# Kernel tuning notes

Hardware: AMD Instinct MI355X
Metric: run time of the kernel (lower is better)

The kernel has to match this reference:

```python
import jax, jax.numpy as jnp
import numpy as np

GROUP_SIZE = 128


def setup_inputs() -> dict:
    key = jax.random.key(0)
    k1, k2, k3 = jax.random.split(key, 3)
    B, S, IN, OUT = 4, 8192, 1024, 1024
    x = jax.random.normal(k1, (B, S, IN), dtype=jnp.float32)
    weight = jax.random.normal(k2, (OUT, IN), dtype=jnp.float32) * 0.02
    bias = jax.random.normal(k3, (OUT,), dtype=jnp.float32) * 0.01
    return {"x": x, "weight": weight, "bias": bias}


def reference(x, weight, bias):
    """Quantized int8 path: quantize() + _forward_int8 of OneBitLinear.

    - weights binarized to +/-1 int8 (sign, with 0 -> -1, matching
      sign().clamp(min=0) bit packing then 2*bit-1)
    - per-group weight scales = group absmax, stored fp16 (as in quantize())
    - activations dynamically quantized per-token to int8
    - int32-accumulated GEMM, rescaled by x_scale * mean group scale per row
    """
    out_f, in_f = weight.shape
    ng = in_f // GROUP_SIZE
    w_g = weight.reshape(out_f, ng, GROUP_SIZE)
    # per-group absmax scales, cast fp16 -> fp32 to mimic fp16 storage
    scales = jnp.maximum(jnp.max(jnp.abs(w_g), axis=-1), 1e-8)
    scales = scales.astype(jnp.float16).astype(jnp.float32)  # [O, ng]
    # +/-1 int8 weights (sign>0 -> +1, else -1; zero maps to -1 like the packer)
    w_int8 = jnp.where(weight > 0, 1, -1).astype(jnp.int8)  # [O, I]

    # dynamic per-token activation quantization
    x_f = x.reshape(-1, in_f)  # [BT, I]
    x_scale = jnp.maximum(jnp.max(jnp.abs(x_f), axis=1, keepdims=True), 1e-8) / 127.0
    x_int8 = jnp.clip(jnp.round(x_f / x_scale), -128, 127).astype(jnp.int8)

    # int8 GEMM with int32 accumulation
    out_i32 = jnp.matmul(
        x_int8.astype(jnp.int32), w_int8.T.astype(jnp.int32)
    )  # [BT, O]

    w_scale_per_row = jnp.mean(scales, axis=1)  # [O]
    out_f32 = out_i32.astype(jnp.float32) * x_scale * w_scale_per_row[None, :]
    out_f32 = out_f32 + bias[None, :]
    return out_f32.reshape(*x.shape[:-1], out_f)
```

## Files before the change

kernel.cpp:

```cpp
#include <hip/hip_runtime.h>
#include <hip/hip_fp16.h>

#define K_DIM 1024
#define N_DIM 1024

typedef int v4i __attribute__((ext_vector_type(4)));

__device__ __forceinline__ void async_load16(const void* g, void* l) {
    __builtin_amdgcn_global_load_lds(
        (const __attribute__((address_space(1))) unsigned int*)g,
        (__attribute__((address_space(3))) unsigned int*)l,
        16, 0, 0);
}

#define BAR() do { asm volatile("" ::: "memory"); \
                   __builtin_amdgcn_s_barrier();  \
                   asm volatile("" ::: "memory"); } while (0)

__global__ __launch_bounds__(256) void prep_quant(const float* __restrict__ w,
                                                  const float* __restrict__ x,
                                                  signed char* __restrict__ wq,
                                                  float* __restrict__ wscale,
                                                  signed char* __restrict__ xq,
                                                  float* __restrict__ xs) {
    const int lane = threadIdx.x & 63;
    if (blockIdx.x < 256) {
        const int row = blockIdx.x * 4 + (threadIdx.x >> 6);
        const float4* wr = (const float4*)(w + (size_t)row * K_DIM);
        float4 v[4];
#pragma unroll
        for (int j = 0; j < 4; ++j) v[j] = wr[lane * 4 + j];

        float g = 0.f;
#pragma unroll
        for (int j = 0; j < 4; ++j) {
            g = fmaxf(g, fabsf(v[j].x)); g = fmaxf(g, fabsf(v[j].y));
            g = fmaxf(g, fabsf(v[j].z)); g = fmaxf(g, fabsf(v[j].w));
        }
        g = fmaxf(g, __shfl_xor(g, 1, 64));
        g = fmaxf(g, __shfl_xor(g, 2, 64));
        g = fmaxf(g, __shfl_xor(g, 4, 64));
        const float s = __half2float(__float2half(fmaxf(g, 1e-8f)));
        float t = s;
        t += __shfl_xor(t, 8, 64);
        t += __shfl_xor(t, 16, 64);
        t += __shfl_xor(t, 32, 64);
        if (lane == 0) wscale[row] = t * 0.125f;

        int pk[4];
#pragma unroll
        for (int j = 0; j < 4; ++j) {
            const int b0 = (v[j].x > 0.f) ? 1 : -1;
            const int b1 = (v[j].y > 0.f) ? 1 : -1;
            const int b2 = (v[j].z > 0.f) ? 1 : -1;
            const int b3 = (v[j].w > 0.f) ? 1 : -1;
            pk[j] = (b0 & 255) | ((b1 & 255) << 8) | ((b2 & 255) << 16) | (b3 << 24);
        }
        *(int4*)(wq + (size_t)row * K_DIM + lane * 16) = make_int4(pk[0], pk[1], pk[2], pk[3]);
    } else {
        const int row = (blockIdx.x - 256) * 4 + (threadIdx.x >> 6);
        const float4* xr = (const float4*)(x + (size_t)row * K_DIM);
        float4 v[4];
#pragma unroll
        for (int j = 0; j < 4; ++j) v[j] = xr[lane * 4 + j];

        float am = 0.f;
#pragma unroll
        for (int j = 0; j < 4; ++j) {
            am = fmaxf(am, fabsf(v[j].x)); am = fmaxf(am, fabsf(v[j].y));
            am = fmaxf(am, fabsf(v[j].z)); am = fmaxf(am, fabsf(v[j].w));
        }
#pragma unroll
        for (int off = 32; off >= 1; off >>= 1) am = fmaxf(am, __shfl_xor(am, off, 64));
        const float scale = fmaxf(am, 1e-8f) / 127.f;
        const float inv   = 1.0f / scale;

        int pk[4];
#pragma unroll
        for (int j = 0; j < 4; ++j) {
            const int b0 = (int)fminf(fmaxf(rintf(v[j].x * inv), -128.f), 127.f);
            const int b1 = (int)fminf(fmaxf(rintf(v[j].y * inv), -128.f), 127.f);
            const int b2 = (int)fminf(fmaxf(rintf(v[j].z * inv), -128.f), 127.f);
            const int b3 = (int)fminf(fmaxf(rintf(v[j].w * inv), -128.f), 127.f);
            pk[j] = (b0 & 255) | ((b1 & 255) << 8) | ((b2 & 255) << 16) | (b3 << 24);
        }
        *(int4*)(xq + (size_t)row * K_DIM + lane * 16) = make_int4(pk[0], pk[1], pk[2], pk[3]);
        if (lane == 0) xs[row] = scale;
    }
}

__global__ __launch_bounds__(256, 4) void gemm_i8(const signed char* __restrict__ A,
                                                  const signed char* __restrict__ Bw,
                                                  const float* __restrict__ xs,
                                                  const float* __restrict__ wscale,
                                                  const float* __restrict__ bias,
                                                  float* __restrict__ out) {
    __shared__ __align__(16) signed char As[2][128 * 64];

    const int tid  = threadIdx.x;
    const int lane = tid & 63;
    const int wave = tid >> 6;
    const int wm = wave >> 1;
    const int wn = wave & 1;

    const int bid = blockIdx.x;
    const int xcd = bid & 7;
    const int q   = bid >> 3;
    const int mT  = xcd * 32 + (q >> 3);
    const int nT  = q & 7;
    const size_t mBase = (size_t)mT * 128;
    const int    nBase = nT * 128;

    const int srow = tid >> 2;
    const int scol = ((tid & 3) ^ (srow & 3)) * 16;
    const int soff = tid * 16;
    const signed char* Ag = A + (mBase + srow) * K_DIM + scol;

#define STAGE(b, kt) do {                                                \
        const int _ko = (kt) * 64;                                       \
        async_load16(Ag + _ko,                      As[b] + soff);       \
        async_load16(Ag + (size_t)64 * K_DIM + _ko, As[b] + 4096 + soff);\
    } while (0)

    v4i acc[4][4] = {};
    const int r16 = lane & 15;
    const int g   = lane >> 4;
    const int co  = (g ^ (r16 & 3)) * 16;

    const signed char* Bgf = Bw + (size_t)(nBase + wn * 64 + r16) * K_DIM + g * 16;

    STAGE(0, 0);

    for (int t = 0; t < 16; ++t) {
        asm volatile("s_waitcnt vmcnt(0)" ::: "memory");
        BAR();

        v4i bf[4];
#pragma unroll
        for (int nf = 0; nf < 4; ++nf)
            bf[nf] = *(const v4i*)(Bgf + (size_t)nf * (16 * K_DIM) + t * 64);

        if (t < 15) STAGE((t + 1) & 1, t + 1);

        const signed char* Ab = As[t & 1];
        v4i af[4];
#pragma unroll
        for (int mf = 0; mf < 4; ++mf)
            af[mf] = *(const v4i*)(Ab + ((wm * 64 + mf * 16 + r16) << 6) + co);

#pragma unroll
        for (int mf = 0; mf < 4; ++mf)
#pragma unroll
            for (int nf = 0; nf < 4; ++nf)
                acc[mf][nf] = __builtin_amdgcn_mfma_i32_16x16x64_i8(
                    af[mf], bf[nf], acc[mf][nf], 0, 0, 0);

        __builtin_amdgcn_sched_barrier(0);
        asm volatile("s_waitcnt lgkmcnt(0)" ::: "memory");
    }
#undef STAGE

    const int cc = r16;
    const int rq = (lane >> 4) * 4;
    float xsr[4][4];
#pragma unroll
    for (int mf = 0; mf < 4; ++mf)
#pragma unroll
        for (int i = 0; i < 4; ++i)
            xsr[mf][i] = xs[mBase + wm * 64 + mf * 16 + rq + i];

#pragma unroll
    for (int nf = 0; nf < 4; ++nf) {
        const int col   = nBase + wn * 64 + nf * 16 + cc;
        const float wsc = wscale[col];
        const float bb  = bias[col];
#pragma unroll
        for (int mf = 0; mf < 4; ++mf) {
#pragma unroll
            for (int i = 0; i < 4; ++i) {
                const size_t row = mBase + wm * 64 + mf * 16 + rq + i;
                out[row * N_DIM + col] = (float)acc[mf][nf][i] * xsr[mf][i] * wsc + bb;
            }
        }
    }
}

extern "C" void kernel_launch(void* const* d_in, const int* in_sizes, int n_in,
                              void* d_out, int out_size, void* d_ws, size_t ws_size,
                              hipStream_t stream) {
    const float* x    = (const float*)d_in[0];
    const float* w    = (const float*)d_in[1];
    const float* bias = (const float*)d_in[2];
    float* out = (float*)d_out;

    const int BT = in_sizes[0] / K_DIM;

    char* ws = (char*)d_ws;
    signed char* xq     = (signed char*)ws;
    float*       xs     = (float*)(ws + (size_t)BT * K_DIM);
    signed char* wq     = (signed char*)(ws + (size_t)BT * K_DIM + (size_t)BT * 4);
    float*       wscale = (float*)((char*)wq + (size_t)N_DIM * K_DIM);

    prep_quant<<<256 + BT / 4, 256, 0, stream>>>(w, x, wq, wscale, xq, xs);
    gemm_i8<<<(BT / 128) * (N_DIM / 128), 256, 0, stream>>>(xq, wq, xs, wscale, bias, out);
}
```

Measured before the change: 301.5 us.

## Stage full weight slab in LDS and stream activations directly from global

The GEMM now loads the whole 128x1024 int8 weight slab for a block into 128KB of dynamic LDS once, using an XOR swizzle, and reads activation fragments straight from global memory into registers. Blocks grow to 512 threads covering a 256x128 output tile, and the per-k-step double-buffered A staging and barriers are gone. This removes the per-iteration synchronization and LDS staging of A, at the cost of exposed global load latency for A with no software prefetch, fewer resident blocks, and a large up-front LDS fill.

New measurement: 304.9 us. About the same (+1.1%).

```diff
diff --git a/kernel.cpp b/kernel.cpp
--- a/kernel.cpp
+++ b/kernel.cpp
@@ -12,10 +12,6 @@
         (__attribute__((address_space(3))) unsigned int*)l,
         16, 0, 0);
 }
-
-#define BAR() do { asm volatile("" ::: "memory"); \
-                   __builtin_amdgcn_s_barrier();  \
-                   asm volatile("" ::: "memory"); } while (0)
 
 __global__ __launch_bounds__(256) void prep_quant(const float* __restrict__ w,
                                                   const float* __restrict__ x,
@@ -89,79 +85,71 @@
     }
 }
 
-__global__ __launch_bounds__(256, 4) void gemm_i8(const signed char* __restrict__ A,
+__global__ __launch_bounds__(512, 2) void gemm_i8(const signed char* __restrict__ A,
                                                   const signed char* __restrict__ Bw,
                                                   const float* __restrict__ xs,
                                                   const float* __restrict__ wscale,
                                                   const float* __restrict__ bias,
                                                   float* __restrict__ out) {
-    __shared__ __align__(16) signed char As[2][128 * 64];
+    extern __shared__ __align__(16) signed char Bl[];
 
     const int tid  = threadIdx.x;
     const int lane = tid & 63;
     const int wave = tid >> 6;
-    const int wm = wave >> 1;
-    const int wn = wave & 1;
+    const int wm   = wave >> 1;
+    const int wn   = wave & 1;
 
     const int bid = blockIdx.x;
     const int xcd = bid & 7;
-    const int q   = bid >> 3;
-    const int mT  = xcd * 32 + (q >> 3);
-    const int nT  = q & 7;
-    const size_t mBase = (size_t)mT * 128;
+    const int u   = bid >> 3;
+    const int mT  = xcd * 16 + (u >> 3);
+    const int nT  = u & 7;
+    const size_t mBase = (size_t)mT * 256;
     const int    nBase = nT * 128;
 
-    const int srow = tid >> 2;
-    const int scol = ((tid & 3) ^ (srow & 3)) * 16;
-    const int soff = tid * 16;
-    const signed char* Ag = A + (mBase + srow) * K_DIM + scol;
-
-#define STAGE(b, kt) do {                                                \
-        const int _ko = (kt) * 64;                                       \
-        async_load16(Ag + _ko,                      As[b] + soff);       \
-        async_load16(Ag + (size_t)64 * K_DIM + _ko, As[b] + 4096 + soff);\
-    } while (0)
-
-    v4i acc[4][4] = {};
+    const int brow   = tid >> 6;
+    const int bchunk = (tid & 63) ^ brow;
+    const signed char* Bg = Bw + (size_t)(nBase + brow) * K_DIM + bchunk * 16;
+#pragma unroll
+    for (int c = 0; c < 16; ++c)
+        async_load16(Bg + (size_t)(c * 8) * K_DIM, Bl + c * 8192 + tid * 16);
+
     const int r16 = lane & 15;
     const int g   = lane >> 4;
-    const int co  = (g ^ (r16 & 3)) * 16;
-
-    const signed char* Bgf = Bw + (size_t)(nBase + wn * 64 + r16) * K_DIM + g * 16;
-
-    STAGE(0, 0);
-
+
+    const signed char* Arow[4];
+#pragma unroll
+    for (int mf = 0; mf < 4; ++mf)
+        Arow[mf] = A + (mBase + wm * 64 + mf * 16 + r16) * (size_t)K_DIM + g * 16;
+
+    const int s7 = r16 & 7;
+    int Bbase[4];
+#pragma unroll
+    for (int nf = 0; nf < 4; ++nf)
+        Bbase[nf] = (wn * 64 + nf * 16 + r16) * 1024;
+
+    __syncthreads();
+
+    v4i acc[4][4] = {};
+
+#pragma unroll
     for (int t = 0; t < 16; ++t) {
-        asm volatile("s_waitcnt vmcnt(0)" ::: "memory");
-        BAR();
-
-        v4i bf[4];
+        v4i af[4], bf[4];
+#pragma unroll
+        for (int mf = 0; mf < 4; ++mf)
+            af[mf] = *(const v4i*)(Arow[mf] + t * 64);
 #pragma unroll
         for (int nf = 0; nf < 4; ++nf)
-            bf[nf] = *(const v4i*)(Bgf + (size_t)nf * (16 * K_DIM) + t * 64);
-
-        if (t < 15) STAGE((t + 1) & 1, t + 1);
-
-        const signed char* Ab = As[t & 1];
-        v4i af[4];
-#pragma unroll
-        for (int mf = 0; mf < 4; ++mf)
-            af[mf] = *(const v4i*)(Ab + ((wm * 64 + mf * 16 + r16) << 6) + co);
-
+            bf[nf] = *(const v4i*)(Bl + Bbase[nf] + (((t * 4 + g) ^ s7) * 16));
 #pragma unroll
         for (int mf = 0; mf < 4; ++mf)
 #pragma unroll
             for (int nf = 0; nf < 4; ++nf)
                 acc[mf][nf] = __builtin_amdgcn_mfma_i32_16x16x64_i8(
                     af[mf], bf[nf], acc[mf][nf], 0, 0, 0);
-
-        __builtin_amdgcn_sched_barrier(0);
-        asm volatile("s_waitcnt lgkmcnt(0)" ::: "memory");
-    }
-#undef STAGE
-
-    const int cc = r16;
-    const int rq = (lane >> 4) * 4;
+    }
+
+    const int rq = g * 4;
     float xsr[4][4];
 #pragma unroll
     for (int mf = 0; mf < 4; ++mf)
@@ -171,7 +159,7 @@
 
 #pragma unroll
     for (int nf = 0; nf < 4; ++nf) {
-        const int col   = nBase + wn * 64 + nf * 16 + cc;
+        const int col   = nBase + wn * 64 + nf * 16 + r16;
         const float wsc = wscale[col];
         const float bb  = bias[col];
 #pragma unroll
@@ -201,6 +189,13 @@
     signed char* wq     = (signed char*)(ws + (size_t)BT * K_DIM + (size_t)BT * 4);
     float*       wscale = (float*)((char*)wq + (size_t)N_DIM * K_DIM);
 
+    static bool s_attr_set = false;
+    if (!s_attr_set) {
+        hipFuncSetAttribute((const void*)gemm_i8,
+                            hipFuncAttributeMaxDynamicSharedMemorySize, 131072);
+        s_attr_set = true;
+    }
+
     prep_quant<<<256 + BT / 4, 256, 0, stream>>>(w, x, wq, wscale, xq, xs);
-    gemm_i8<<<(BT / 128) * (N_DIM / 128), 256, 0, stream>>>(xq, wq, xs, wscale, bias, out);
-}
+    gemm_i8<<<(BT / 256) * (N_DIM / 128), 512, 131072, stream>>>(xq, wq, xs, wscale, bias, out);
+}
```
